# Kernel optimization log

Measured on AMD Instinct MI355X. Metric: run time of the kernel, lower is better.

Reference implementation:

```python
import math
import jax, jax.numpy as jnp
import numpy as np

B, T, C = 4, 2048, 1024
H = 16
D = C // H  # head_dim = 64


def setup_inputs() -> dict:
    key = jax.random.key(0)
    ks = jax.random.split(key, 5)
    scale = 0.02
    return {
        "x": jax.random.normal(ks[0], (B, T, C), dtype=jnp.float32),
        "w_attn": jax.random.normal(ks[1], (C, 3 * C), dtype=jnp.float32) * scale,
        "b_attn": jax.random.normal(ks[2], (3 * C,), dtype=jnp.float32) * scale,
        "w_proj": jax.random.normal(ks[3], (C, C), dtype=jnp.float32) * scale,
        "b_proj": jax.random.normal(ks[4], (C,), dtype=jnp.float32) * scale,
    }


def reference(x, w_attn, b_attn, w_proj, b_proj):
    b, t, c = x.shape
    qkv = x @ w_attn + b_attn                       # [B,T,3C]
    q, k, v = jnp.split(qkv, 3, axis=-1)
    q = q.reshape(b, t, H, D)
    k = k.reshape(b, t, H, D)
    v = v.reshape(b, t, H, D)
    # scores: [B,H,T,T]
    att = jnp.einsum('bthd,bshd->bhts', q, k) * (1.0 / math.sqrt(D))
    causal = jnp.tril(jnp.ones((t, t), dtype=bool))
    att = jnp.where(causal, att, -jnp.inf)
    att = jax.nn.softmax(att, axis=-1)
    y = jnp.einsum('bhts,bshd->bthd', att, v).reshape(b, t, c)
    return y @ w_proj + b_proj
```

## Files before the change

kernel.cpp:

```cpp
#include <hip/hip_runtime.h>

#define BB 4
#define TT 2048
#define CC 1024
#define HH 16
#define DD 64
#define MM (BB*TT)
#define N3 (3*CC)

typedef unsigned short u16;
typedef __attribute__((ext_vector_type(8))) __bf16 bf16x8;
typedef __attribute__((ext_vector_type(4))) float f32x4;
typedef __attribute__((ext_vector_type(8))) u16 u16x8;
typedef __attribute__((ext_vector_type(4))) u16 u16x4;

__device__ __forceinline__ u16 f2bf(float f) {
  return __builtin_bit_cast(u16, (__bf16)f);
}

__device__ __forceinline__ void gload16(const void* g, void* lds) {
  __builtin_amdgcn_global_load_lds(
      (const __attribute__((address_space(1))) void*)g,
      (__attribute__((address_space(3))) void*)lds, 16, 0, 0);
}

__global__ __launch_bounds__(256) void k_cvt(const float* __restrict__ in, u16* __restrict__ out) {
  size_t i = ((size_t)blockIdx.x * 256 + threadIdx.x) * 8;
  f32x4 a = *(const f32x4*)(in + i);
  f32x4 b = *(const f32x4*)(in + i + 4);
  u16x8 o;
  o[0]=f2bf(a[0]); o[1]=f2bf(a[1]); o[2]=f2bf(a[2]); o[3]=f2bf(a[3]);
  o[4]=f2bf(b[0]); o[5]=f2bf(b[1]); o[6]=f2bf(b[2]); o[7]=f2bf(b[3]);
  *(u16x8*)(out + i) = o;
}

__global__ __launch_bounds__(256) void k_tr(const float* __restrict__ in, u16* __restrict__ out,
                                            int R, int Cc) {
  __shared__ float t[32][33];
  int cb = blockIdx.x * 32, rb = blockIdx.y * 32;
  int tx = threadIdx.x, ty = threadIdx.y;
  #pragma unroll
  for (int j = 0; j < 4; ++j)
    t[ty + j*8][tx] = in[(size_t)(rb + ty + j*8) * Cc + cb + tx];
  __syncthreads();
  #pragma unroll
  for (int j = 0; j < 4; ++j)
    out[(size_t)(cb + ty + j*8) * R + rb + tx] = f2bf(t[tx][ty + j*8]);
}

__device__ __forceinline__ void gemm_core(const u16* __restrict__ A, const u16* __restrict__ Bt,
                                          int KDIM, int mbase, int nbase,
                                          u16* As, u16* Bs, f32x4 acc[4][4]) {
  int tid = threadIdx.x;
  int lane = tid & 63;
  int w = tid >> 6;
  int wm = (w >> 1) * 64, wn = (w & 1) * 64;
  int r = lane & 15, kq = (lane >> 4) * 8;
  for (int kb = 0; kb < KDIM; kb += 32) {
    #pragma unroll
    for (int i = 0; i < 2; ++i) {
      int c = tid + 256 * i;
      int row = c >> 2, kc = c & 3;
      gload16(A  + (size_t)(mbase + row) * KDIM + kb + kc * 8, As + c * 8);
      gload16(Bt + (size_t)(nbase + row) * KDIM + kb + kc * 8, Bs + c * 8);
    }
    __syncthreads();
    bf16x8 af[4], bfr[4];
    #pragma unroll
    for (int mi = 0; mi < 4; ++mi) af[mi]  = *(const bf16x8*)&As[(wm + mi*16 + r) * 32 + kq];
    #pragma unroll
    for (int ni = 0; ni < 4; ++ni) bfr[ni] = *(const bf16x8*)&Bs[(wn + ni*16 + r) * 32 + kq];
    #pragma unroll
    for (int mi = 0; mi < 4; ++mi)
      #pragma unroll
      for (int ni = 0; ni < 4; ++ni)
        acc[mi][ni] = __builtin_amdgcn_mfma_f32_16x16x32_bf16(af[mi], bfr[ni], acc[mi][ni], 0, 0, 0);
    __syncthreads();
  }
}

__global__ __launch_bounds__(256) void k_gemm_qkv(const u16* __restrict__ Xb, const u16* __restrict__ WaT,
                                                  const float* __restrict__ b_attn,
                                                  u16* __restrict__ Qh, u16* __restrict__ Kh,
                                                  u16* __restrict__ Vt) {
  __shared__ u16 As[128*32], Bs[128*32];
  f32x4 acc[4][4] = {};
  int mbase = blockIdx.x * 128, nbase = blockIdx.y * 128;
  gemm_core(Xb, WaT, CC, mbase, nbase, As, Bs, acc);
  int lane = threadIdx.x & 63, w = threadIdx.x >> 6;
  int wm = (w >> 1) * 64, wn = (w & 1) * 64;
  int r = lane & 15, g = lane >> 4;
  int which = nbase >> 10;
  if (which < 2) {
    u16* dst = which == 0 ? Qh : Kh;
    #pragma unroll
    for (int mi = 0; mi < 4; ++mi)
      #pragma unroll
      for (int ni = 0; ni < 4; ++ni)
        #pragma unroll
        for (int reg = 0; reg < 4; ++reg) {
          int m = mbase + wm + mi*16 + 4*g + reg;
          int n = nbase + wn + ni*16 + r;
          float v = acc[mi][ni][reg] + b_attn[n];
          int ccol = n & (CC - 1);
          int h = ccol >> 6, d = ccol & 63;
          int bb = m >> 11, t = m & (TT - 1);
          dst[((size_t)(bb*HH + h)*TT + t)*DD + d] = f2bf(v);
        }
  } else {
    #pragma unroll
    for (int mi = 0; mi < 4; ++mi)
      #pragma unroll
      for (int ni = 0; ni < 4; ++ni) {
        int m0 = mbase + wm + mi*16 + 4*g;
        int n = nbase + wn + ni*16 + r;
        float bn = b_attn[n];
        int ccol = n & (CC - 1);
        int h = ccol >> 6, d = ccol & 63;
        int bb = m0 >> 11, t0 = m0 & (TT - 1);
        u16x4 pk;
        #pragma unroll
        for (int reg = 0; reg < 4; ++reg)
          pk[reg] = f2bf(acc[mi][ni][reg] + bn);
        *(u16x4*)&Vt[((size_t)(bb*HH + h)*DD + d)*TT + t0] = pk;
      }
  }
}

__global__ __launch_bounds__(256) void k_attn(const u16* __restrict__ Qh, const u16* __restrict__ Kh,
                                              const u16* __restrict__ Vtg, u16* __restrict__ Yh) {
  __shared__ u16 Ks[2][64*64];
  __shared__ u16 Vs[2][64*64];
  __shared__ u16 Pl[4][32*64];
  int bid = blockIdx.x;
  int bh = (bid & 7) * 8 + (bid >> 6);
  int p  = (bid >> 3) & 7;
  int b = bh >> 4, h = bh & 15;
  int tid = threadIdx.x, lane = tid & 63, w = tid >> 6;
  int r = lane & 15, g = lane >> 4;
  size_t hoff = (size_t)bh * TT * DD;
  u16* pw = Pl[w];

  bf16x8 ones;
  #pragma unroll
  for (int e = 0; e < 8; ++e) ones[e] = (__bf16)1.0f;

  auto STAGE = [&](int buf, int kb) {
    #pragma unroll
    for (int i = 0; i < 2; ++i) {
      int c = tid + 256*i;
      int row = c >> 3, ch = c & 7;
      int chs = ch ^ (row & 7);
      gload16(Kh  + hoff + (size_t)(kb*64 + row)*DD + chs*8, &Ks[buf][c*8]);
      gload16(Vtg + hoff + (size_t)row*TT + kb*64 + chs*8,   &Vs[buf][c*8]);
    }
  };

  for (int ph = 0; ph < 2; ++ph) {
    int qt = ph == 0 ? (15 - p) : p;
    int qrow0 = qt*128 + w*32;
    int nkb = 2*qt + 2;

    bf16x8 qf[2][2];
    #pragma unroll
    for (int ni = 0; ni < 2; ++ni)
      #pragma unroll
      for (int ks = 0; ks < 2; ++ks)
        qf[ni][ks] = *(const bf16x8*)(Qh + hoff + (size_t)(qrow0 + ni*16 + r)*DD + ks*32 + g*8);

    f32x4 o[2][4] = {};
    f32x4 lacc[2] = {};

    STAGE(0, 0);
    __syncthreads();
    int buf = 0;

    for (int kb = 0; kb < nkb; ++kb) {
      if (kb + 1 < nkb) STAGE(buf ^ 1, kb + 1);

      if (kb*64 <= qrow0 + 31) {
        f32x4 s[2][4] = {};
        __builtin_amdgcn_s_setprio(1);
        #pragma unroll
        for (int nf = 0; nf < 4; ++nf)
          #pragma unroll
          for (int ks = 0; ks < 2; ++ks) {
            bf16x8 kf = *(const bf16x8*)&Ks[buf][(nf*16 + r)*64 + (((ks*4 + g) ^ (r & 7)) << 3)];
            #pragma unroll
            for (int ni = 0; ni < 2; ++ni)
              s[ni][nf] = __builtin_amdgcn_mfma_f32_16x16x32_bf16(kf, qf[ni][ks], s[ni][nf], 0, 0, 0);
          }
        __builtin_amdgcn_s_setprio(0);
        bool need_mask = (kb*64 + 63 > qrow0);
        #pragma unroll
        for (int ni = 0; ni < 2; ++ni)
          #pragma unroll
          for (int nf = 0; nf < 4; ++nf)
            #pragma unroll
            for (int reg = 0; reg < 4; ++reg) {
              float sv = s[ni][nf][reg] * 0.18033688011112043f;
              if (need_mask) {
                int key = kb*64 + nf*16 + 4*g + reg;
                int qrow = qrow0 + ni*16 + r;
                sv = (key > qrow) ? -1e30f : sv;
              }
              s[ni][nf][reg] = __builtin_amdgcn_exp2f(sv);
            }
        #pragma unroll
        for (int ni = 0; ni < 2; ++ni)
          #pragma unroll
          for (int nf = 0; nf < 4; ++nf) {
            int qh_ = ni*16 + r;
            int chunk = 2*nf + (g >> 1);
            u16x4 pk;
            #pragma unroll
            for (int reg = 0; reg < 4; ++reg) pk[reg] = f2bf(s[ni][nf][reg]);
            *(u16x4*)&pw[qh_*64 + ((chunk ^ (qh_ & 7)) << 3) + ((g & 1) << 2)] = pk;
          }
        __builtin_amdgcn_s_setprio(1);
        #pragma unroll
        for (int ks = 0; ks < 2; ++ks) {
          bf16x8 pb[2];
          #pragma unroll
          for (int ni = 0; ni < 2; ++ni)
            pb[ni] = *(const bf16x8*)&pw[(ni*16 + r)*64 + (((ks*4 + g) ^ (r & 7)) << 3)];
          #pragma unroll
          for (int nf2 = 0; nf2 < 4; ++nf2) {
            bf16x8 vf = *(const bf16x8*)&Vs[buf][(nf2*16 + r)*64 + (((ks*4 + g) ^ (r & 7)) << 3)];
            #pragma unroll
            for (int ni = 0; ni < 2; ++ni)
              o[ni][nf2] = __builtin_amdgcn_mfma_f32_16x16x32_bf16(vf, pb[ni], o[ni][nf2], 0, 0, 0);
          }
          #pragma unroll
          for (int ni = 0; ni < 2; ++ni)
            lacc[ni] = __builtin_amdgcn_mfma_f32_16x16x32_bf16(ones, pb[ni], lacc[ni], 0, 0, 0);
        }
        __builtin_amdgcn_s_setprio(0);
      }
      __syncthreads();
      buf ^= 1;
    }

    #pragma unroll
    for (int ni = 0; ni < 2; ++ni) {
      float inv = 1.0f / lacc[ni][0];
      int t = qrow0 + ni*16 + r;
      #pragma unroll
      for (int nf2 = 0; nf2 < 4; ++nf2) {
        u16x4 pk;
        #pragma unroll
        for (int reg = 0; reg < 4; ++reg)
          pk[reg] = f2bf(o[ni][nf2][reg] * inv);
        *(u16x4*)&Yh[((size_t)b*TT + t)*CC + h*DD + nf2*16 + 4*g] = pk;
      }
    }
  }
}

__global__ __launch_bounds__(256) void k_gemm_proj(const u16* __restrict__ Yh, const u16* __restrict__ WpT,
                                                   const float* __restrict__ b_proj,
                                                   float* __restrict__ out) {
  __shared__ u16 As[128*32], Bs[128*32];
  f32x4 acc[4][4] = {};
  int mbase = blockIdx.x * 128, nbase = blockIdx.y * 128;
  gemm_core(Yh, WpT, CC, mbase, nbase, As, Bs, acc);
  int lane = threadIdx.x & 63, w = threadIdx.x >> 6;
  int wm = (w >> 1) * 64, wn = (w & 1) * 64;
  int r = lane & 15, g = lane >> 4;
  #pragma unroll
  for (int mi = 0; mi < 4; ++mi)
    #pragma unroll
    for (int ni = 0; ni < 4; ++ni)
      #pragma unroll
      for (int reg = 0; reg < 4; ++reg) {
        int m = mbase + wm + mi*16 + 4*g + reg;
        int n = nbase + wn + ni*16 + r;
        out[(size_t)m*CC + n] = acc[mi][ni][reg] + b_proj[n];
      }
}

extern "C" void kernel_launch(void* const* d_in, const int* in_sizes, int n_in,
                              void* d_out, int out_size, void* d_ws, size_t ws_size,
                              hipStream_t stream) {
  const float* x      = (const float*)d_in[0];
  const float* w_attn = (const float*)d_in[1];
  const float* b_attn = (const float*)d_in[2];
  const float* w_proj = (const float*)d_in[3];
  const float* b_proj = (const float*)d_in[4];
  float* out = (float*)d_out;

  u16* Xb  = (u16*)d_ws;
  u16* WaT = Xb  + (size_t)MM*CC;
  u16* WpT = WaT + (size_t)N3*CC;
  u16* Qh  = WpT + (size_t)CC*CC;
  u16* Kh  = Qh  + (size_t)BB*HH*TT*DD;
  u16* Vt  = Kh  + (size_t)BB*HH*TT*DD;
  u16* Yh  = Vt  + (size_t)BB*HH*TT*DD;

  k_cvt<<<dim3(MM*CC/(256*8)), dim3(256), 0, stream>>>(x, Xb);
  k_tr <<<dim3(N3/32, CC/32), dim3(32,8), 0, stream>>>(w_attn, WaT, CC, N3);
  k_tr <<<dim3(CC/32, CC/32), dim3(32,8), 0, stream>>>(w_proj, WpT, CC, CC);
  k_gemm_qkv<<<dim3(MM/128, N3/128), dim3(256), 0, stream>>>(Xb, WaT, b_attn, Qh, Kh, Vt);
  k_attn<<<dim3(BB*HH*8), dim3(256), 0, stream>>>(Qh, Kh, Vt, Yh);
  k_gemm_proj<<<dim3(MM/128, CC/128), dim3(256), 0, stream>>>(Yh, WpT, b_proj, out);
}
```

Measured before the change: 185.8 us.

## Rewrite GEMMs with 3-stage LDS ring, swizzle, 128x256 tiles and XCD grid mapping

Replaces the synchronous BK=32 GEMM core with a triple-buffered ring of BK=64 stages loaded via global_load_lds, using vmcnt waits and a single barrier per step to overlap loads with MFMA. LDS chunks are XOR-swizzled to avoid bank conflicts, blocks grow to 512 threads with 128x256 tiles, and a 1D grid is remapped so neighbouring tiles share an XCD for L2 reuse. This is meant to cut memory stalls and barrier overhead in the QKV and projection GEMMs. It costs much more LDS per block (144KB), which limits occupancy.

```diff
diff --git a/kernel.cpp b/kernel.cpp
--- a/kernel.cpp
+++ b/kernel.cpp
@@ -7,6 +7,7 @@
 #define DD 64
 #define MM (BB*TT)
 #define N3 (3*CC)
+#define NTK 16
 
 typedef unsigned short u16;
 typedef __attribute__((ext_vector_type(8))) __bf16 bf16x8;
@@ -48,47 +49,88 @@
     out[(size_t)(cb + ty + j*8) * R + rb + tx] = f2bf(t[tx][ty + j*8]);
 }
 
-__device__ __forceinline__ void gemm_core(const u16* __restrict__ A, const u16* __restrict__ Bt,
-                                          int KDIM, int mbase, int nbase,
-                                          u16* As, u16* Bs, f32x4 acc[4][4]) {
+__device__ __forceinline__ void gemm_ring(const u16* __restrict__ A, const u16* __restrict__ Bt,
+                                          int mbase, int nbase,
+                                          u16 (*As)[128*64], u16 (*Bs)[256*64],
+                                          f32x4 acc[4][4]) {
   int tid = threadIdx.x;
   int lane = tid & 63;
-  int w = tid >> 6;
-  int wm = (w >> 1) * 64, wn = (w & 1) * 64;
-  int r = lane & 15, kq = (lane >> 4) * 8;
-  for (int kb = 0; kb < KDIM; kb += 32) {
+  int wid = tid >> 6;
+  int wm = (wid >> 2) * 64, wn = (wid & 3) * 64;
+  int r = lane & 15, g = lane >> 4;
+
+  auto STAGE = [&](int sl, int u) {
+    int kb = u * 64;
     #pragma unroll
     for (int i = 0; i < 2; ++i) {
-      int c = tid + 256 * i;
-      int row = c >> 2, kc = c & 3;
-      gload16(A  + (size_t)(mbase + row) * KDIM + kb + kc * 8, As + c * 8);
-      gload16(Bt + (size_t)(nbase + row) * KDIM + kb + kc * 8, Bs + c * 8);
-    }
-    __syncthreads();
-    bf16x8 af[4], bfr[4];
-    #pragma unroll
-    for (int mi = 0; mi < 4; ++mi) af[mi]  = *(const bf16x8*)&As[(wm + mi*16 + r) * 32 + kq];
-    #pragma unroll
-    for (int ni = 0; ni < 4; ++ni) bfr[ni] = *(const bf16x8*)&Bs[(wn + ni*16 + r) * 32 + kq];
-    #pragma unroll
-    for (int mi = 0; mi < 4; ++mi)
+      int c = tid + 512*i;
+      int row = c >> 3, ch = c & 7;
+      int chs = ch ^ (row & 7);
+      gload16(A + (size_t)(mbase + row)*CC + kb + chs*8, &As[sl][c*8]);
+    }
+    #pragma unroll
+    for (int i = 0; i < 4; ++i) {
+      int c = tid + 512*i;
+      int row = c >> 3, ch = c & 7;
+      int chs = ch ^ (row & 7);
+      gload16(Bt + (size_t)(nbase + row)*CC + kb + chs*8, &Bs[sl][c*8]);
+    }
+  };
+
+  STAGE(0, 0);
+  STAGE(1, 1);
+  asm volatile("s_waitcnt vmcnt(6)" ::: "memory");
+  __builtin_amdgcn_s_barrier();
+
+  int sl = 0;
+  for (int u = 0; u < NTK; ++u) {
+    int s2 = sl + 2; if (s2 >= 3) s2 -= 3;
+    if (u + 2 < NTK) STAGE(s2, u + 2);
+
+    bf16x8 af[2][4], bfr[2][4];
+    #pragma unroll
+    for (int ks = 0; ks < 2; ++ks) {
+      #pragma unroll
+      for (int mi = 0; mi < 4; ++mi)
+        af[ks][mi] = *(const bf16x8*)&As[sl][(wm + mi*16 + r)*64 + (((ks*4 + g) ^ (r & 7)) << 3)];
       #pragma unroll
       for (int ni = 0; ni < 4; ++ni)
-        acc[mi][ni] = __builtin_amdgcn_mfma_f32_16x16x32_bf16(af[mi], bfr[ni], acc[mi][ni], 0, 0, 0);
-    __syncthreads();
+        bfr[ks][ni] = *(const bf16x8*)&Bs[sl][(wn + ni*16 + r)*64 + (((ks*4 + g) ^ (r & 7)) << 3)];
+    }
+    #pragma unroll
+    for (int ks = 0; ks < 2; ++ks)
+      #pragma unroll
+      for (int mi = 0; mi < 4; ++mi)
+        #pragma unroll
+        for (int ni = 0; ni < 4; ++ni)
+          acc[mi][ni] = __builtin_amdgcn_mfma_f32_16x16x32_bf16(af[ks][mi], bfr[ks][ni], acc[mi][ni], 0, 0, 0);
+
+    if (u + 2 < NTK) asm volatile("s_waitcnt vmcnt(6)" ::: "memory");
+    else             asm volatile("s_waitcnt vmcnt(0)" ::: "memory");
+    __builtin_amdgcn_s_barrier();
+    ++sl; if (sl >= 3) sl -= 3;
   }
 }
 
-__global__ __launch_bounds__(256) void k_gemm_qkv(const u16* __restrict__ Xb, const u16* __restrict__ WaT,
+__device__ __forceinline__ void grid_map(int bid, int& bx, int& by) {
+  int xcd = bid & 7;
+  int idx = bid >> 3;
+  bx = xcd * 8 + (idx & 7);
+  by = idx >> 3;
+}
+
+__global__ __launch_bounds__(512) void k_gemm_qkv(const u16* __restrict__ Xb, const u16* __restrict__ WaT,
                                                   const float* __restrict__ b_attn,
                                                   u16* __restrict__ Qh, u16* __restrict__ Kh,
                                                   u16* __restrict__ Vt) {
-  __shared__ u16 As[128*32], Bs[128*32];
+  __shared__ u16 As[3][128*64];
+  __shared__ u16 Bs[3][256*64];
   f32x4 acc[4][4] = {};
-  int mbase = blockIdx.x * 128, nbase = blockIdx.y * 128;
-  gemm_core(Xb, WaT, CC, mbase, nbase, As, Bs, acc);
-  int lane = threadIdx.x & 63, w = threadIdx.x >> 6;
-  int wm = (w >> 1) * 64, wn = (w & 1) * 64;
+  int bx, by; grid_map(blockIdx.x, bx, by);
+  int mbase = bx * 128, nbase = by * 256;
+  gemm_ring(Xb, WaT, mbase, nbase, As, Bs, acc);
+  int lane = threadIdx.x & 63, wid = threadIdx.x >> 6;
+  int wm = (wid >> 2) * 64, wn = (wid & 3) * 64;
   int r = lane & 15, g = lane >> 4;
   int which = nbase >> 10;
   if (which < 2) {
@@ -125,6 +167,30 @@
         *(u16x4*)&Vt[((size_t)(bb*HH + h)*DD + d)*TT + t0] = pk;
       }
   }
+}
+
+__global__ __launch_bounds__(512) void k_gemm_proj(const u16* __restrict__ Yh, const u16* __restrict__ WpT,
+                                                   const float* __restrict__ b_proj,
+                                                   float* __restrict__ out) {
+  __shared__ u16 As[3][128*64];
+  __shared__ u16 Bs[3][256*64];
+  f32x4 acc[4][4] = {};
+  int bx, by; grid_map(blockIdx.x, bx, by);
+  int mbase = bx * 128, nbase = by * 256;
+  gemm_ring(Yh, WpT, mbase, nbase, As, Bs, acc);
+  int lane = threadIdx.x & 63, wid = threadIdx.x >> 6;
+  int wm = (wid >> 2) * 64, wn = (wid & 3) * 64;
+  int r = lane & 15, g = lane >> 4;
+  #pragma unroll
+  for (int mi = 0; mi < 4; ++mi)
+    #pragma unroll
+    for (int ni = 0; ni < 4; ++ni)
+      #pragma unroll
+      for (int reg = 0; reg < 4; ++reg) {
+        int m = mbase + wm + mi*16 + 4*g + reg;
+        int n = nbase + wn + ni*16 + r;
+        out[(size_t)m*CC + n] = acc[mi][ni][reg] + b_proj[n];
+      }
 }
 
 __global__ __launch_bounds__(256) void k_attn(const u16* __restrict__ Qh, const u16* __restrict__ Kh,
@@ -257,28 +323,6 @@
   }
 }
 
-__global__ __launch_bounds__(256) void k_gemm_proj(const u16* __restrict__ Yh, const u16* __restrict__ WpT,
-                                                   const float* __restrict__ b_proj,
-                                                   float* __restrict__ out) {
-  __shared__ u16 As[128*32], Bs[128*32];
-  f32x4 acc[4][4] = {};
-  int mbase = blockIdx.x * 128, nbase = blockIdx.y * 128;
-  gemm_core(Yh, WpT, CC, mbase, nbase, As, Bs, acc);
-  int lane = threadIdx.x & 63, w = threadIdx.x >> 6;
-  int wm = (w >> 1) * 64, wn = (w & 1) * 64;
-  int r = lane & 15, g = lane >> 4;
-  #pragma unroll
-  for (int mi = 0; mi < 4; ++mi)
-    #pragma unroll
-    for (int ni = 0; ni < 4; ++ni)
-      #pragma unroll
-      for (int reg = 0; reg < 4; ++reg) {
-        int m = mbase + wm + mi*16 + 4*g + reg;
-        int n = nbase + wn + ni*16 + r;
-        out[(size_t)m*CC + n] = acc[mi][ni][reg] + b_proj[n];
-      }
-}
-
 extern "C" void kernel_launch(void* const* d_in, const int* in_sizes, int n_in,
                               void* d_out, int out_size, void* d_ws, size_t ws_size,
                               hipStream_t stream) {
@@ -300,7 +344,7 @@
   k_cvt<<<dim3(MM*CC/(256*8)), dim3(256), 0, stream>>>(x, Xb);
   k_tr <<<dim3(N3/32, CC/32), dim3(32,8), 0, stream>>>(w_attn, WaT, CC, N3);
   k_tr <<<dim3(CC/32, CC/32), dim3(32,8), 0, stream>>>(w_proj, WpT, CC, CC);
-  k_gemm_qkv<<<dim3(MM/128, N3/128), dim3(256), 0, stream>>>(Xb, WaT, b_attn, Qh, Kh, Vt);
+  k_gemm_qkv<<<dim3((MM/128)*(N3/256)), dim3(512), 0, stream>>>(Xb, WaT, b_attn, Qh, Kh, Vt);
   k_attn<<<dim3(BB*HH*8), dim3(256), 0, stream>>>(Qh, Kh, Vt, Yh);
-  k_gemm_proj<<<dim3(MM/128, CC/128), dim3(256), 0, stream>>>(Yh, WpT, b_proj, out);
-}
+  k_gemm_proj<<<dim3((MM/128)*(CC/256)), dim3(512), 0, stream>>>(Yh, WpT, b_proj, out);
+}
```

Result: no change. 188.8 us (+1.6%).
